# Optimization experiments

Hardware: AMD Instinct MI355X
Metric: run time of the kernel (lower is better)

Reference implementation:

```python
import jax, jax.numpy as jnp
import numpy as np

EPS = 1e-8
CLAMP = 1.0 - 1e-5
C = 1.0  # curvature


def _norm(x):
    return jnp.sqrt(jnp.sum(x * x, axis=-1, keepdims=True))


def clamp_to_ball(x, c=C):
    max_norm = CLAMP / c ** 0.5
    n = jnp.maximum(_norm(x), EPS)
    scale = jnp.where(n > max_norm, max_norm / n, 1.0)
    return x * scale


def logmap0(x, c=C):
    n = jnp.maximum(_norm(x), EPS)
    sc = c ** 0.5
    a = jnp.minimum(sc * n, 1.0 - EPS)
    return jnp.arctanh(a) / (sc * n) * x


def expmap0(v, c=C):
    n = jnp.maximum(_norm(v), EPS)
    sc = c ** 0.5
    t = jnp.minimum(sc * n, 15.0)
    return clamp_to_ball(jnp.tanh(t) * v / (sc * n), c)


def mobius_add(x, y, c=C):
    x2 = jnp.sum(x * x, -1, keepdims=True)
    y2 = jnp.sum(y * y, -1, keepdims=True)
    xy = jnp.sum(x * y, -1, keepdims=True)
    num = (1 + 2 * c * xy + c * y2) * x + (1 - c * x2) * y
    den = 1 + 2 * c * xy + c * c * x2 * y2
    return clamp_to_ball(num / jnp.maximum(den, EPS), c)


def hyp_linear(x, W, b, c=C):
    out = expmap0(logmap0(x, c) @ W.T, c)
    bias_ball = expmap0(b[None, :], c)
    return mobius_add(out, jnp.broadcast_to(bias_ball, out.shape), c)


def pairwise_poincare_dist(Q, K, c=C):
    # Q, K: [B, h, T, dk]. Distance d(q,k) = 2/sqrt(c) * atanh(sqrt(c)*||(-q) (+) k||).
    # ||num||^2 of mobius_add(-q, k) depends only on scalars |q|^2, |k|^2, q.k,
    # so we avoid the (B,h,T,T,dk) expansion while computing identical math.
    q2 = jnp.sum(Q * Q, -1)[..., :, None]          # [B,h,T,1]
    k2 = jnp.sum(K * K, -1)[..., None, :]          # [B,h,1,T]
    xy = -jnp.einsum('bhtd,bhsd->bhts', Q, K)      # (-q).k
    A = 1 + 2 * c * xy + c * k2
    Bc = 1 - c * q2
    num2 = A * A * q2 + Bc * Bc * k2 + 2 * A * Bc * xy
    den = jnp.maximum(1 + 2 * c * xy + c * c * q2 * k2, EPS)
    n = jnp.sqrt(jnp.maximum(num2, 0.0)) / den
    n = jnp.minimum(n, CLAMP / c ** 0.5)           # clamp_to_ball on the diff vector
    n = jnp.minimum(n, 1.0 - EPS)                  # .clamp(max=1-EPS)
    sc = c ** 0.5
    return 2.0 / sc * jnp.arctanh(sc * n)


def setup_inputs() -> dict:
    key = jax.random.key(0)
    ks = jax.random.split(key, 10)
    B, T, d = 4, 1024, 512
    x = expmap0(0.05 * jax.random.normal(ks[0], (B, T, d), jnp.float32))
    a = (6.0 / (d + d)) ** 0.5  # xavier uniform bound
    def w(k):
        return jax.random.uniform(k, (d, d), jnp.float32, -a, a)
    return {
        'x': x,
        'Wq': w(ks[1]), 'bq': 0.01 * jax.random.normal(ks[2], (d,), jnp.float32),
        'Wk': w(ks[3]), 'bk': 0.01 * jax.random.normal(ks[4], (d,), jnp.float32),
        'Wv': w(ks[5]), 'bv': 0.01 * jax.random.normal(ks[6], (d,), jnp.float32),
        'Wo': w(ks[7]), 'bo': 0.01 * jax.random.normal(ks[8], (d,), jnp.float32),
    }


def reference(x, Wq, bq, Wk, bk, Wv, bv, Wo, bo):
    B, T, d = x.shape
    h = 8
    dk = d // h
    x_eucl = logmap0(x, C)
    Q = hyp_linear(x, Wq, bq, C)
    K = hyp_linear(x, Wk, bk, C)
    V = x_eucl @ Wv.T + bv
    Q = Q.reshape(B, T, h, dk).transpose(0, 2, 1, 3)
    K = K.reshape(B, T, h, dk).transpose(0, 2, 1, 3)
    V = V.reshape(B, T, h, dk).transpose(0, 2, 1, 3)
    dists = pairwise_poincare_dist(Q, K, C)        # [B,h,T,T]
    scores = -dists / (dk ** 0.5)
    attn = jax.nn.softmax(scores, axis=-1)
    out = jnp.einsum('bhts,bhsd->bhtd', attn, V)
    out = out.transpose(0, 2, 1, 3).reshape(B, T, d)
    return out @ Wo.T + bo
```

## Files before the change

kernel.cpp:

```cpp
#include <hip/hip_runtime.h>
#include <math.h>

#define EPSF   1e-8f
#define CLAMPF 0.99999f

typedef __attribute__((ext_vector_type(8))) short bf16x8;
typedef __attribute__((ext_vector_type(4))) float f32x4;
#define MFMA16(a,b,c) __builtin_amdgcn_mfma_f32_16x16x32_bf16(a,b,c,0,0,0)

__device__ __forceinline__ unsigned cvt_pk_bf16(float lo, float hi) {
  unsigned r;
  asm("v_cvt_pk_bf16_f32 %0, %1, %2" : "=v"(r) : "v"(lo), "v"(hi));
  return r;
}

__device__ __forceinline__ float wave_sum64(float v) {
  v += __shfl_xor(v, 1, 64);
  v += __shfl_xor(v, 2, 64);
  v += __shfl_xor(v, 4, 64);
  v += __shfl_xor(v, 8, 64);
  v += __shfl_xor(v, 16, 64);
  v += __shfl_xor(v, 32, 64);
  return v;
}

__global__ __launch_bounds__(256) void prep_logmap(const float* __restrict__ x,
                                                   const float* __restrict__ Wq,
                                                   const float* __restrict__ Wk,
                                                   const float* __restrict__ Wv,
                                                   const float* __restrict__ Wo,
                                                   const float* __restrict__ bq,
                                                   const float* __restrict__ bk,
                                                   short* __restrict__ xe,
                                                   short* __restrict__ Wqbf,
                                                   short* __restrict__ Wkbf,
                                                   short* __restrict__ Wvbf,
                                                   short* __restrict__ Wobf,
                                                   float* __restrict__ bb) {
  const int id = blockIdx.x;
  const int t = threadIdx.x;
  __shared__ float red[4];
  if (id < 4096) {
    float2 v = ((const float2*)(x + (size_t)id * 512))[t];
    float s = wave_sum64(v.x * v.x + v.y * v.y);
    if ((t & 63) == 0) red[t >> 6] = s;
    __syncthreads();
    float n2 = red[0] + red[1] + red[2] + red[3];
    float n = sqrtf(n2);
    float nm = fmaxf(n, EPSF);
    float a = fminf(nm, 1.0f);
    float at = 0.5f * logf((1.f + a) / (1.f - a));
    float sc = at / nm;
    ((unsigned*)(xe + (size_t)id * 512))[t] = cvt_pk_bf16(v.x * sc, v.y * sc);
    return;
  }
  const int wid = id - 4096;
  if (wid < 512) {
    const int which = wid >> 7, chunk = wid & 127;
    const float* src; short* dst;
    switch (which) {
      case 0: src = Wq; dst = Wqbf; break;
      case 1: src = Wk; dst = Wkbf; break;
      case 2: src = Wv; dst = Wvbf; break;
      default: src = Wo; dst = Wobf; break;
    }
    const int idx = chunk * 2048 + t * 8;
    float4 a = *(const float4*)(src + idx);
    float4 b2 = *(const float4*)(src + idx + 4);
    union { int4 v; unsigned u[4]; } o;
    o.u[0] = cvt_pk_bf16(a.x, a.y);
    o.u[1] = cvt_pk_bf16(a.z, a.w);
    o.u[2] = cvt_pk_bf16(b2.x, b2.y);
    o.u[3] = cvt_pk_bf16(b2.z, b2.w);
    *(int4*)(dst + idx) = o.v;
    return;
  }
  const int which = wid - 512;
  const float* b = which ? bk : bq;
  float* o = bb + (size_t)which * 520;
  float2 v = ((const float2*)b)[t];
  float s = wave_sum64(v.x * v.x + v.y * v.y);
  if ((t & 63) == 0) red[t >> 6] = s;
  __syncthreads();
  float n2 = red[0] + red[1] + red[2] + red[3];
  float n = sqrtf(n2);
  float nm = fmaxf(n, EPSF);
  float tt = fminf(nm, 15.f);
  float f = tanhf(tt) / nm;
  float on = f * nm;
  if (on > CLAMPF) f *= CLAMPF / on;
  ((float2*)o)[t] = make_float2(f * v.x, f * v.y);
  if (t == 0) o[512] = f * f * n2;
}

template <int VT>
__device__ __forceinline__ void gemm_core(const short* __restrict__ A,
                                          const short* __restrict__ W,
                                          const float* __restrict__ bias,
                                          void* __restrict__ outp,
                                          int bx, int by) {
  __shared__ __align__(16) short As[64][72];
  __shared__ __align__(16) short Ws[64][72];
  const int t = threadIdx.x;
  const int wave = t >> 6, lane = t & 63, lg = lane >> 4, lr = lane & 15;
  const int mh = wave & 1, nh = wave >> 1;
  f32x4 z = {0.f, 0.f, 0.f, 0.f};
  f32x4 acc00 = z, acc01 = z, acc10 = z, acc11 = z;
  const int srow = t >> 2, sc = (t & 3) * 16;
  const short* Ab = A + (size_t)(by * 64 + srow) * 512 + sc;
  const short* Wb = W + (size_t)(bx * 64 + srow) * 512 + sc;

  int4 ra0 = *(const int4*)(Ab);
  int4 ra1 = *(const int4*)(Ab + 8);
  int4 rw0 = *(const int4*)(Wb);
  int4 rw1 = *(const int4*)(Wb + 8);

  for (int kt = 0; kt < 512; kt += 64) {
    __syncthreads();
    *(int4*)&As[srow][sc] = ra0;
    *(int4*)&As[srow][sc + 8] = ra1;
    *(int4*)&Ws[srow][sc] = rw0;
    *(int4*)&Ws[srow][sc + 8] = rw1;
    __syncthreads();
    if (kt < 448) {
      ra0 = *(const int4*)(Ab + kt + 64);
      ra1 = *(const int4*)(Ab + kt + 72);
      rw0 = *(const int4*)(Wb + kt + 64);
      rw1 = *(const int4*)(Wb + kt + 72);
    }
#pragma unroll
    for (int kk = 0; kk < 2; ++kk) {
      bf16x8 af0 = *(const bf16x8*)&As[mh * 32 + lr][kk * 32 + lg * 8];
      bf16x8 af1 = *(const bf16x8*)&As[mh * 32 + 16 + lr][kk * 32 + lg * 8];
      bf16x8 bf0 = *(const bf16x8*)&Ws[nh * 32 + lr][kk * 32 + lg * 8];
      bf16x8 bf1 = *(const bf16x8*)&Ws[nh * 32 + 16 + lr][kk * 32 + lg * 8];
      acc00 = MFMA16(af0, bf0, acc00);
      acc01 = MFMA16(af0, bf1, acc01);
      acc10 = MFMA16(af1, bf0, acc10);
      acc11 = MFMA16(af1, bf1, acc11);
    }
  }

  if (VT == 0) {
    float* out = (float*)outp;
    float b0 = 0.f, b1 = 0.f;
    if (bias) { b0 = bias[bx * 64 + nh * 32 + lr]; b1 = bias[bx * 64 + nh * 32 + 16 + lr]; }
#pragma unroll
    for (int r = 0; r < 4; ++r) {
      size_t row0 = (size_t)(by * 64 + mh * 32 + lg * 4 + r);
      size_t row1 = row0 + 16;
      out[row0 * 512 + bx * 64 + nh * 32 + lr] = acc00[r] + b0;
      out[row0 * 512 + bx * 64 + nh * 32 + 16 + lr] = acc01[r] + b1;
      out[row1 * 512 + bx * 64 + nh * 32 + lr] = acc10[r] + b0;
      out[row1 * 512 + bx * 64 + nh * 32 + 16 + lr] = acc11[r] + b1;
    }
  } else {
    short* vt = (short*)outp;
    const int bidx = by >> 4;
    const int trow0 = (by & 15) * 64 + mh * 32 + lg * 4;
    const int c0 = bx * 64 + nh * 32 + lr;
    const int c1 = c0 + 16;
    const float b0 = bias[c0], b1 = bias[c1];
    size_t base0 = ((size_t)(bidx * 8 + (c0 >> 6)) * 64 + (c0 & 63)) * 1024;
    size_t base1 = ((size_t)(bidx * 8 + (c1 >> 6)) * 64 + (c1 & 63)) * 1024;
    uint2 pk;
    pk.x = cvt_pk_bf16(acc00[0] + b0, acc00[1] + b0);
    pk.y = cvt_pk_bf16(acc00[2] + b0, acc00[3] + b0);
    *(uint2*)(vt + base0 + trow0) = pk;
    pk.x = cvt_pk_bf16(acc01[0] + b1, acc01[1] + b1);
    pk.y = cvt_pk_bf16(acc01[2] + b1, acc01[3] + b1);
    *(uint2*)(vt + base1 + trow0) = pk;
    pk.x = cvt_pk_bf16(acc10[0] + b0, acc10[1] + b0);
    pk.y = cvt_pk_bf16(acc10[2] + b0, acc10[3] + b0);
    *(uint2*)(vt + base0 + trow0 + 16) = pk;
    pk.x = cvt_pk_bf16(acc11[0] + b1, acc11[1] + b1);
    pk.y = cvt_pk_bf16(acc11[2] + b1, acc11[3] + b1);
    *(uint2*)(vt + base1 + trow0 + 16) = pk;
  }
}

__global__ __launch_bounds__(256) void gemm_qkv(const short* __restrict__ A,
                                                const short* __restrict__ Wq,
                                                const short* __restrict__ Wk,
                                                const short* __restrict__ Wv,
                                                const float* __restrict__ bv,
                                                float* __restrict__ Qo,
                                                float* __restrict__ Ko,
                                                short* __restrict__ Vt) {
  switch (blockIdx.z) {
    case 0: gemm_core<0>(A, Wq, nullptr, Qo, blockIdx.x, blockIdx.y); break;
    case 1: gemm_core<0>(A, Wk, nullptr, Ko, blockIdx.x, blockIdx.y); break;
    default: gemm_core<1>(A, Wv, bv, Vt, blockIdx.x, blockIdx.y); break;
  }
}

__global__ __launch_bounds__(256) void gemm_bf(const short* __restrict__ A,
                                               const short* __restrict__ W,
                                               const float* __restrict__ bias,
                                               float* __restrict__ out) {
  gemm_core<0>(A, W, bias, out, blockIdx.x, blockIdx.y);
}

__global__ __launch_bounds__(256) void hyp_epilogue_v3(const float* __restrict__ Qb,
                                                       const float* __restrict__ Kb,
                                                       const float* __restrict__ bbase,
                                                       short* __restrict__ Qbf,
                                                       short* __restrict__ Kbf,
                                                       float* __restrict__ q2h,
                                                       float* __restrict__ k2h) {
  const int row = blockIdx.x;
  const int which = blockIdx.y;
  const float* Y = which ? Kb : Qb;
  const float* bb = bbase + (size_t)which * 520;
  short* Ybf = which ? Kbf : Qbf;
  float* y2h = which ? k2h : q2h;
  const int t = threadIdx.x;
  float2 y = ((const float2*)(Y + (size_t)row * 512))[t];
  float2 w = ((const float2*)bb)[t];
  __shared__ float red[8];
  float sn = wave_sum64(y.x * y.x + y.y * y.y);
  float sd = wave_sum64(y.x * w.x + y.y * w.y);
  if ((t & 63) == 0) { red[t >> 6] = sn; red[4 + (t >> 6)] = sd; }
  __syncthreads();
  float n2 = red[0] + red[1] + red[2] + red[3];
  float dt = red[4] + red[5] + red[6] + red[7];
  float y2 = bb[512];
  float n = sqrtf(n2);
  float nm = fmaxf(n, EPSF);
  float tt = fminf(nm, 15.f);
  float f = tanhf(tt) / nm;
  float on = f * nm;
  if (on > CLAMPF) f *= CLAMPF / on;
  float x2 = f * f * n2;
  float xy = f * dt;
  float A = 1.f + 2.f * xy + y2;
  float Bc = 1.f - x2;
  float den = fmaxf(1.f + 2.f * xy + x2 * y2, EPSF);
  float num2 = A * A * x2 + Bc * Bc * y2 + 2.f * A * Bc * xy;
  float nn = sqrtf(fmaxf(num2, 0.f)) / den;
  float nnm = fmaxf(nn, EPSF);
  float s2 = (nnm > CLAMPF) ? (CLAMPF / nnm) : 1.f;
  float g = s2 / den;
  float ox = g * (A * f * y.x + Bc * w.x);
  float oy = g * (A * f * y.y + Bc * w.y);
  ((unsigned*)(Ybf + (size_t)row * 512))[t] = cvt_pk_bf16(ox, oy);
  float hs = ox * ox + oy * oy;
  hs += __shfl_xor(hs, 1, 64);
  hs += __shfl_xor(hs, 2, 64);
  hs += __shfl_xor(hs, 4, 64);
  hs += __shfl_xor(hs, 8, 64);
  hs += __shfl_xor(hs, 16, 64);
  if ((t & 31) == 0) y2h[(size_t)(t >> 5) * 4096 + row] = hs;
}

__global__ __launch_bounds__(256) void attn_mfma(const short* __restrict__ Qbf,
                                                 const short* __restrict__ Kbf,
                                                 const float* __restrict__ q2h,
                                                 const float* __restrict__ k2h,
                                                 const short* __restrict__ Vt,
                                                 short* __restrict__ Obf) {
  __shared__ __align__(16) short Qs[32][72];
  __shared__ __align__(16) short Ks[64][72];
  __shared__ __align__(16) short Vs[64][72];
  __shared__ __align__(16) short Ps[32][72];
  __shared__ float k2s[64];
  __shared__ float lsl[4][32];

  const int t = threadIdx.x;
  const int id = blockIdx.x;
  const int qt = id >> 5;
  const int pr = (((id >> 3) & 3) << 3) | (id & 7);
  const int hd = pr & 7, b = pr >> 3;

  const int wave = t >> 6, lane = t & 63, lg = lane >> 4, lr = lane & 15;
  const size_t hbase = (size_t)b * 1024 * 512 + (size_t)hd * 64;
  const size_t vtb = (size_t)(b * 8 + hd) * 64 * 1024;
  const int sr = t >> 3, sc8 = (t & 7) * 8;

  *(int4*)&Qs[sr][sc8] = *(const int4*)(Qbf + hbase + (size_t)(qt * 32 + sr) * 512 + sc8);
  __syncthreads();

  bf16x8 qf[2][2];
#pragma unroll
  for (int m = 0; m < 2; ++m)
#pragma unroll
    for (int kk = 0; kk < 2; ++kk)
      qf[m][kk] = *(const bf16x8*)&Qs[m * 16 + lr][kk * 32 + lg * 8];

  float q2m[2], bc2m[2], q2p1m2[2];
#pragma unroll
  for (int m = 0; m < 2; ++m) {
    float q2 = q2h[(size_t)hd * 4096 + b * 1024 + qt * 32 + m * 16 + lr];
    q2m[m] = q2;
    float bc = 1.f - q2;
    bc2m[m] = bc * bc;
    q2p1m2[m] = -2.f * (1.f + q2);
  }

  f32x4 z = {0.f, 0.f, 0.f, 0.f};
  f32x4 accT0 = z, accT1 = z;
  float lsm[2] = {0.f, 0.f};

  const short* kp = Kbf + hbase + (size_t)sr * 512 + sc8;
  const short* vp = Vt + vtb + (size_t)sr * 1024 + sc8;
  const float* k2p = k2h + (size_t)hd * 4096 + b * 1024 + t;

  int4 ka = *(const int4*)kp;
  int4 kb2 = *(const int4*)(kp + 32 * 512);
  int4 va = *(const int4*)vp;
  int4 vb2 = *(const int4*)(vp + 32 * 1024);
  float k2r = 0.f;
  if (t < 64) k2r = *k2p;

  for (int kt = 0; kt < 16; ++kt) {
    __syncthreads();
    *(int4*)&Ks[sr][sc8] = ka;
    *(int4*)&Ks[sr + 32][sc8] = kb2;
    *(int4*)&Vs[sr][sc8] = va;
    *(int4*)&Vs[sr + 32][sc8] = vb2;
    if (t < 64) k2s[t] = k2r;
    __syncthreads();
    if (kt < 15) {
      kp += 64 * 512; vp += 64; k2p += 64;
      ka = *(const int4*)kp;
      kb2 = *(const int4*)(kp + 32 * 512);
      va = *(const int4*)vp;
      vb2 = *(const int4*)(vp + 32 * 1024);
      if (t < 64) k2r = *k2p;
    }

    bf16x8 kf0 = *(const bf16x8*)&Ks[wave * 16 + lr][0 + lg * 8];
    bf16x8 kf1 = *(const bf16x8*)&Ks[wave * 16 + lr][32 + lg * 8];
    f32x4 s0 = z, s1 = z;
    s0 = MFMA16(kf0, qf[0][0], s0);
    s0 = MFMA16(kf1, qf[0][1], s0);
    s1 = MFMA16(kf0, qf[1][0], s1);
    s1 = MFMA16(kf1, qf[1][1], s1);

    float k2v[4], k2p1[4], k2p1sq[4];
#pragma unroll
    for (int r = 0; r < 4; ++r) {
      k2v[r] = k2s[wave * 16 + lg * 4 + r];
      k2p1[r] = 1.f + k2v[r];
      k2p1sq[r] = k2p1[r] * k2p1[r];
    }
#pragma unroll
    for (int m = 0; m < 2; ++m) {
      f32x4 sv = m ? s1 : s0;
      float p[4];
#pragma unroll
      for (int r = 0; r < 4; ++r) {
        float d = sv[r];
        float c1 = q2p1m2[m] * k2p1[r];
        float c0 = fmaf(q2m[m], k2p1sq[r], bc2m[m] * k2v[r]);
        float num2 = fmaf(d, fmaf(4.f, d, c1), c0);
        float den = fmaf(-2.f, d, fmaf(q2m[m], k2v[r], 1.f));
        num2 = fmaxf(num2, 0.f);
        den = fmaxf(den, EPSF);
        float sq = __builtin_amdgcn_sqrtf(num2);
        float u = (den - sq) * __builtin_amdgcn_rcpf(den + sq);
        u = fmaxf(u, 5.000025e-6f);
        p[r] = __builtin_amdgcn_exp2f(0.125f * __builtin_amdgcn_logf(u));
      }
      lsm[m] += (p[0] + p[1]) + (p[2] + p[3]);
      uint2 pk;
      pk.x = cvt_pk_bf16(p[0], p[1]);
      pk.y = cvt_pk_bf16(p[2], p[3]);
      *(uint2*)&Ps[m * 16 + lr][wave * 16 + lg * 4] = pk;
    }
    __syncthreads();

    bf16x8 vf0 = *(const bf16x8*)&Vs[wave * 16 + lr][0 + lg * 8];
    bf16x8 vf1 = *(const bf16x8*)&Vs[wave * 16 + lr][32 + lg * 8];
    bf16x8 pa00 = *(const bf16x8*)&Ps[lr][0 + lg * 8];
    bf16x8 pa01 = *(const bf16x8*)&Ps[lr][32 + lg * 8];
    bf16x8 pa10 = *(const bf16x8*)&Ps[16 + lr][0 + lg * 8];
    bf16x8 pa11 = *(const bf16x8*)&Ps[16 + lr][32 + lg * 8];
    accT0 = MFMA16(vf0, pa00, accT0);
    accT0 = MFMA16(vf1, pa01, accT0);
    accT1 = MFMA16(vf0, pa10, accT1);
    accT1 = MFMA16(vf1, pa11, accT1);
  }

#pragma unroll
  for (int m = 0; m < 2; ++m) {
    float v = lsm[m];
    v += __shfl_xor(v, 16, 64);
    v += __shfl_xor(v, 32, 64);
    lsm[m] = v;
  }
  if (lg == 0) {
    lsl[wave][lr] = lsm[0];
    lsl[wave][16 + lr] = lsm[1];
  }
  __syncthreads();

  float inv0 = 1.f / (lsl[0][lr] + lsl[1][lr] + lsl[2][lr] + lsl[3][lr]);
  float inv1 = 1.f / (lsl[0][16 + lr] + lsl[1][16 + lr] + lsl[2][16 + lr] + lsl[3][16 + lr]);

  short* ob0 = Obf + ((size_t)b * 1024 + qt * 32 + lr) * 512 + hd * 64 + wave * 16 + lg * 4;
  short* ob1 = Obf + ((size_t)b * 1024 + qt * 32 + 16 + lr) * 512 + hd * 64 + wave * 16 + lg * 4;
  *(unsigned*)(ob0)     = cvt_pk_bf16(accT0[0] * inv0, accT0[1] * inv0);
  *(unsigned*)(ob0 + 2) = cvt_pk_bf16(accT0[2] * inv0, accT0[3] * inv0);
  *(unsigned*)(ob1)     = cvt_pk_bf16(accT1[0] * inv1, accT1[1] * inv1);
  *(unsigned*)(ob1 + 2) = cvt_pk_bf16(accT1[2] * inv1, accT1[3] * inv1);
}

extern "C" void kernel_launch(void* const* d_in, const int* in_sizes, int n_in,
                              void* d_out, int out_size, void* d_ws, size_t ws_size,
                              hipStream_t stream) {
  const float* x  = (const float*)d_in[0];
  const float* Wq = (const float*)d_in[1];
  const float* bq = (const float*)d_in[2];
  const float* Wk = (const float*)d_in[3];
  const float* bk = (const float*)d_in[4];
  const float* Wv = (const float*)d_in[5];
  const float* bv = (const float*)d_in[6];
  const float* Wo = (const float*)d_in[7];
  const float* bo = (const float*)d_in[8];
  float* out = (float*)d_out;
  float* ws  = (float*)d_ws;

  const size_t M1 = 1048576ull;
  float* Qb    = ws;
  float* Kb    = ws + 2 * M1;
  short* Vt    = (short*)(ws + 4 * M1);
  short* xe_bf = (short*)(ws + 5 * M1);
  short* Qbf   = (short*)(ws + 5 * M1);
  short* Wqbf  = (short*)(ws + 6 * M1);
  short* Wkbf  = (short*)(ws + 6 * M1 + 131072);
  short* Wvbf  = (short*)(ws + 6 * M1 + 262144);
  short* Wobf  = (short*)(ws + 6 * M1 + 393216);
  short* attn_out = (short*)(ws + 6 * M1 + 524288);
  short* Kbf = (short*)out;
  float* bb  = out + M1;
  float* q2h = out + M1 + 2048;
  float* k2h = out + M1 + 2048 + 32768;

  hipLaunchKernelGGL(prep_logmap, dim3(4610), dim3(256), 0, stream,
                     x, Wq, Wk, Wv, Wo, bq, bk, xe_bf, Wqbf, Wkbf, Wvbf, Wobf, bb);

  hipLaunchKernelGGL(gemm_qkv, dim3(8, 64, 3), dim3(256), 0, stream,
                     xe_bf, Wqbf, Wkbf, Wvbf, bv, Qb, Kb, Vt);

  hipLaunchKernelGGL(hyp_epilogue_v3, dim3(4096, 2), dim3(256), 0, stream,
                     Qb, Kb, bb, Qbf, Kbf, q2h, k2h);

  hipLaunchKernelGGL(attn_mfma, dim3(1024), dim3(256), 0, stream,
                     Qbf, Kbf, q2h, k2h, Vt, attn_out);

  hipLaunchKernelGGL(gemm_bf, dim3(8, 64), dim3(256), 0, stream, attn_out, Wobf, bo, out);
}
```

Before: 82.94 us.

## Restructure attention kernel as register-resident split-K with no shared-memory staging

The attention kernel now gives each wave a 16-row query half and a 512-key half, loads K, V and k2 fragments straight from global memory into registers with one-step prefetch, and feeds the probability tile to the PV MFMA directly from registers through a permuted K row order. This removes the per-iteration LDS staging and the three block barriers per key tile. The two key halves are merged once at the end through shared memory. The cost is redundant global loads across waves, uncoalesced fragment loads, and a final reduction step; launch bounds now ask for 4 blocks per CU.

```diff
diff --git a/kernel.cpp b/kernel.cpp
--- a/kernel.cpp
+++ b/kernel.cpp
@@ -253,157 +253,151 @@
   if ((t & 31) == 0) y2h[(size_t)(t >> 5) * 4096 + row] = hs;
 }
 
-__global__ __launch_bounds__(256) void attn_mfma(const short* __restrict__ Qbf,
-                                                 const short* __restrict__ Kbf,
-                                                 const float* __restrict__ q2h,
-                                                 const float* __restrict__ k2h,
-                                                 const short* __restrict__ Vt,
-                                                 short* __restrict__ Obf) {
-  __shared__ __align__(16) short Qs[32][72];
-  __shared__ __align__(16) short Ks[64][72];
-  __shared__ __align__(16) short Vs[64][72];
-  __shared__ __align__(16) short Ps[32][72];
-  __shared__ float k2s[64];
-  __shared__ float lsl[4][32];
+__global__ __launch_bounds__(256, 4) void attn_mfma_v2(const short* __restrict__ Qbf,
+                                                       const short* __restrict__ Kbf,
+                                                       const float* __restrict__ q2h,
+                                                       const float* __restrict__ k2h,
+                                                       const short* __restrict__ Vt,
+                                                       short* __restrict__ Obf) {
+  __shared__ __align__(16) float Ls[2][16][68];
+  __shared__ float lsb[2][16];
 
   const int t = threadIdx.x;
   const int id = blockIdx.x;
   const int qt = id >> 5;
   const int pr = (((id >> 3) & 3) << 3) | (id & 7);
   const int hd = pr & 7, b = pr >> 3;
-
   const int wave = t >> 6, lane = t & 63, lg = lane >> 4, lr = lane & 15;
-  const size_t hbase = (size_t)b * 1024 * 512 + (size_t)hd * 64;
-  const size_t vtb = (size_t)(b * 8 + hd) * 64 * 1024;
-  const int sr = t >> 3, sc8 = (t & 7) * 8;
-
-  *(int4*)&Qs[sr][sc8] = *(const int4*)(Qbf + hbase + (size_t)(qt * 32 + sr) * 512 + sc8);
-  __syncthreads();
-
-  bf16x8 qf[2][2];
-#pragma unroll
-  for (int m = 0; m < 2; ++m)
-#pragma unroll
-    for (int kk = 0; kk < 2; ++kk)
-      qf[m][kk] = *(const bf16x8*)&Qs[m * 16 + lr][kk * 32 + lg * 8];
-
-  float q2m[2], bc2m[2], q2p1m2[2];
-#pragma unroll
-  for (int m = 0; m < 2; ++m) {
-    float q2 = q2h[(size_t)hd * 4096 + b * 1024 + qt * 32 + m * 16 + lr];
-    q2m[m] = q2;
-    float bc = 1.f - q2;
-    bc2m[m] = bc * bc;
-    q2p1m2[m] = -2.f * (1.f + q2);
-  }
+  const int qh = wave & 1, kh = wave >> 1;
+
+  const size_t qrow = (size_t)(b * 1024 + qt * 32 + qh * 16 + lr);
+  const bf16x8 qf0 = *(const bf16x8*)(Qbf + qrow * 512 + hd * 64 + lg * 8);
+  const bf16x8 qf1 = *(const bf16x8*)(Qbf + qrow * 512 + hd * 64 + 32 + lg * 8);
+
+  const float q2 = q2h[(size_t)hd * 4096 + b * 1024 + qt * 32 + qh * 16 + lr];
+  const float bc = 1.f - q2;
+  const float bc2 = bc * bc;
+  const float q2p1m2 = -2.f * (1.f + q2);
+
+  const int permA = (lr & 3) | ((lr >> 2) << 3);
+  const short* kpA = Kbf + (size_t)(b * 1024 + kh * 512 + permA) * 512 + hd * 64 + lg * 8;
+  const short* kpB = kpA + 4 * 512;
+  const short* vp  = Vt + ((size_t)(b * 8 + hd) * 64 + lr) * 1024 + kh * 512 + lg * 8;
+  const float* c2p = k2h + (size_t)hd * 4096 + b * 1024 + kh * 512 + lg * 8;
 
   f32x4 z = {0.f, 0.f, 0.f, 0.f};
-  f32x4 accT0 = z, accT1 = z;
-  float lsm[2] = {0.f, 0.f};
-
-  const short* kp = Kbf + hbase + (size_t)sr * 512 + sc8;
-  const short* vp = Vt + vtb + (size_t)sr * 1024 + sc8;
-  const float* k2p = k2h + (size_t)hd * 4096 + b * 1024 + t;
-
-  int4 ka = *(const int4*)kp;
-  int4 kb2 = *(const int4*)(kp + 32 * 512);
-  int4 va = *(const int4*)vp;
-  int4 vb2 = *(const int4*)(vp + 32 * 1024);
-  float k2r = 0.f;
-  if (t < 64) k2r = *k2p;
-
-  for (int kt = 0; kt < 16; ++kt) {
-    __syncthreads();
-    *(int4*)&Ks[sr][sc8] = ka;
-    *(int4*)&Ks[sr + 32][sc8] = kb2;
-    *(int4*)&Vs[sr][sc8] = va;
-    *(int4*)&Vs[sr + 32][sc8] = vb2;
-    if (t < 64) k2s[t] = k2r;
-    __syncthreads();
-    if (kt < 15) {
-      kp += 64 * 512; vp += 64; k2p += 64;
-      ka = *(const int4*)kp;
-      kb2 = *(const int4*)(kp + 32 * 512);
-      va = *(const int4*)vp;
-      vb2 = *(const int4*)(vp + 32 * 1024);
-      if (t < 64) k2r = *k2p;
-    }
-
-    bf16x8 kf0 = *(const bf16x8*)&Ks[wave * 16 + lr][0 + lg * 8];
-    bf16x8 kf1 = *(const bf16x8*)&Ks[wave * 16 + lr][32 + lg * 8];
-    f32x4 s0 = z, s1 = z;
-    s0 = MFMA16(kf0, qf[0][0], s0);
-    s0 = MFMA16(kf1, qf[0][1], s0);
-    s1 = MFMA16(kf0, qf[1][0], s1);
-    s1 = MFMA16(kf1, qf[1][1], s1);
-
-    float k2v[4], k2p1[4], k2p1sq[4];
+  f32x4 acc0 = z, acc1 = z, acc2 = z, acc3 = z;
+  float ls = 0.f;
+
+  bf16x8 kA0 = *(const bf16x8*)(kpA);
+  bf16x8 kA1 = *(const bf16x8*)(kpA + 32);
+  bf16x8 kB0 = *(const bf16x8*)(kpB);
+  bf16x8 kB1 = *(const bf16x8*)(kpB + 32);
+  bf16x8 v0 = *(const bf16x8*)(vp);
+  bf16x8 v1 = *(const bf16x8*)(vp + 16 * 1024);
+  bf16x8 v2 = *(const bf16x8*)(vp + 32 * 1024);
+  bf16x8 v3 = *(const bf16x8*)(vp + 48 * 1024);
+  f32x4 c2a = *(const f32x4*)(c2p);
+  f32x4 c2b = *(const f32x4*)(c2p + 4);
+
+  for (int tt = 0; tt < 16; ++tt) {
+    f32x4 sA = MFMA16(kA1, qf1, z);
+    sA = MFMA16(kA0, qf0, sA);
+    f32x4 sB = MFMA16(kB1, qf1, z);
+    sB = MFMA16(kB0, qf0, sB);
+
+    kpA += 32 * 512; kpB += 32 * 512;
+    bf16x8 nA0 = *(const bf16x8*)(kpA);
+    bf16x8 nA1 = *(const bf16x8*)(kpA + 32);
+    bf16x8 nB0 = *(const bf16x8*)(kpB);
+    bf16x8 nB1 = *(const bf16x8*)(kpB + 32);
+
+    float pA[4], pB[4];
 #pragma unroll
     for (int r = 0; r < 4; ++r) {
-      k2v[r] = k2s[wave * 16 + lg * 4 + r];
-      k2p1[r] = 1.f + k2v[r];
-      k2p1sq[r] = k2p1[r] * k2p1[r];
+      float d = sA[r];
+      float k2v = c2a[r];
+      float k2p1 = 1.f + k2v;
+      float c1 = q2p1m2 * k2p1;
+      float c0 = fmaf(q2, k2p1 * k2p1, bc2 * k2v);
+      float num2 = fmaxf(fmaf(d, fmaf(4.f, d, c1), c0), 0.f);
+      float den = fmaxf(fmaf(-2.f, d, fmaf(q2, k2v, 1.f)), EPSF);
+      float sq = __builtin_amdgcn_sqrtf(num2);
+      float u = fmaxf((den - sq) * __builtin_amdgcn_rcpf(den + sq), 5.000025e-6f);
+      pA[r] = __builtin_amdgcn_exp2f(0.125f * __builtin_amdgcn_logf(u));
     }
 #pragma unroll
-    for (int m = 0; m < 2; ++m) {
-      f32x4 sv = m ? s1 : s0;
-      float p[4];
-#pragma unroll
-      for (int r = 0; r < 4; ++r) {
-        float d = sv[r];
-        float c1 = q2p1m2[m] * k2p1[r];
-        float c0 = fmaf(q2m[m], k2p1sq[r], bc2m[m] * k2v[r]);
-        float num2 = fmaf(d, fmaf(4.f, d, c1), c0);
-        float den = fmaf(-2.f, d, fmaf(q2m[m], k2v[r], 1.f));
-        num2 = fmaxf(num2, 0.f);
-        den = fmaxf(den, EPSF);
-        float sq = __builtin_amdgcn_sqrtf(num2);
-        float u = (den - sq) * __builtin_amdgcn_rcpf(den + sq);
-        u = fmaxf(u, 5.000025e-6f);
-        p[r] = __builtin_amdgcn_exp2f(0.125f * __builtin_amdgcn_logf(u));
-      }
-      lsm[m] += (p[0] + p[1]) + (p[2] + p[3]);
-      uint2 pk;
-      pk.x = cvt_pk_bf16(p[0], p[1]);
-      pk.y = cvt_pk_bf16(p[2], p[3]);
-      *(uint2*)&Ps[m * 16 + lr][wave * 16 + lg * 4] = pk;
-    }
-    __syncthreads();
-
-    bf16x8 vf0 = *(const bf16x8*)&Vs[wave * 16 + lr][0 + lg * 8];
-    bf16x8 vf1 = *(const bf16x8*)&Vs[wave * 16 + lr][32 + lg * 8];
-    bf16x8 pa00 = *(const bf16x8*)&Ps[lr][0 + lg * 8];
-    bf16x8 pa01 = *(const bf16x8*)&Ps[lr][32 + lg * 8];
-    bf16x8 pa10 = *(const bf16x8*)&Ps[16 + lr][0 + lg * 8];
-    bf16x8 pa11 = *(const bf16x8*)&Ps[16 + lr][32 + lg * 8];
-    accT0 = MFMA16(vf0, pa00, accT0);
-    accT0 = MFMA16(vf1, pa01, accT0);
-    accT1 = MFMA16(vf0, pa10, accT1);
-    accT1 = MFMA16(vf1, pa11, accT1);
-  }
-
-#pragma unroll
-  for (int m = 0; m < 2; ++m) {
-    float v = lsm[m];
-    v += __shfl_xor(v, 16, 64);
-    v += __shfl_xor(v, 32, 64);
-    lsm[m] = v;
-  }
-  if (lg == 0) {
-    lsl[wave][lr] = lsm[0];
-    lsl[wave][16 + lr] = lsm[1];
+    for (int r = 0; r < 4; ++r) {
+      float d = sB[r];
+      float k2v = c2b[r];
+      float k2p1 = 1.f + k2v;
+      float c1 = q2p1m2 * k2p1;
+      float c0 = fmaf(q2, k2p1 * k2p1, bc2 * k2v);
+      float num2 = fmaxf(fmaf(d, fmaf(4.f, d, c1), c0), 0.f);
+      float den = fmaxf(fmaf(-2.f, d, fmaf(q2, k2v, 1.f)), EPSF);
+      float sq = __builtin_amdgcn_sqrtf(num2);
+      float u = fmaxf((den - sq) * __builtin_amdgcn_rcpf(den + sq), 5.000025e-6f);
+      pB[r] = __builtin_amdgcn_exp2f(0.125f * __builtin_amdgcn_logf(u));
+    }
+    ls += (pA[0] + pA[1] + pA[2] + pA[3]) + (pB[0] + pB[1] + pB[2] + pB[3]);
+
+    c2p += 32;
+    f32x4 nc2a = *(const f32x4*)(c2p);
+    f32x4 nc2b = *(const f32x4*)(c2p + 4);
+
+    union { unsigned u[4]; bf16x8 v; } pf;
+    pf.u[0] = cvt_pk_bf16(pA[0], pA[1]);
+    pf.u[1] = cvt_pk_bf16(pA[2], pA[3]);
+    pf.u[2] = cvt_pk_bf16(pB[0], pB[1]);
+    pf.u[3] = cvt_pk_bf16(pB[2], pB[3]);
+
+    acc0 = MFMA16(v0, pf.v, acc0);
+    acc1 = MFMA16(v1, pf.v, acc1);
+    acc2 = MFMA16(v2, pf.v, acc2);
+    acc3 = MFMA16(v3, pf.v, acc3);
+
+    vp += 32;
+    v0 = *(const bf16x8*)(vp);
+    v1 = *(const bf16x8*)(vp + 16 * 1024);
+    v2 = *(const bf16x8*)(vp + 32 * 1024);
+    v3 = *(const bf16x8*)(vp + 48 * 1024);
+
+    kA0 = nA0; kA1 = nA1; kB0 = nB0; kB1 = nB1;
+    c2a = nc2a; c2b = nc2b;
+  }
+
+  ls += __shfl_xor(ls, 16, 64);
+  ls += __shfl_xor(ls, 32, 64);
+
+  if (kh == 1) {
+    *(f32x4*)&Ls[qh][lr][lg * 4]      = acc0;
+    *(f32x4*)&Ls[qh][lr][16 + lg * 4] = acc1;
+    *(f32x4*)&Ls[qh][lr][32 + lg * 4] = acc2;
+    *(f32x4*)&Ls[qh][lr][48 + lg * 4] = acc3;
+    if (lg == 0) lsb[qh][lr] = ls;
   }
   __syncthreads();
-
-  float inv0 = 1.f / (lsl[0][lr] + lsl[1][lr] + lsl[2][lr] + lsl[3][lr]);
-  float inv1 = 1.f / (lsl[0][16 + lr] + lsl[1][16 + lr] + lsl[2][16 + lr] + lsl[3][16 + lr]);
-
-  short* ob0 = Obf + ((size_t)b * 1024 + qt * 32 + lr) * 512 + hd * 64 + wave * 16 + lg * 4;
-  short* ob1 = Obf + ((size_t)b * 1024 + qt * 32 + 16 + lr) * 512 + hd * 64 + wave * 16 + lg * 4;
-  *(unsigned*)(ob0)     = cvt_pk_bf16(accT0[0] * inv0, accT0[1] * inv0);
-  *(unsigned*)(ob0 + 2) = cvt_pk_bf16(accT0[2] * inv0, accT0[3] * inv0);
-  *(unsigned*)(ob1)     = cvt_pk_bf16(accT1[0] * inv1, accT1[1] * inv1);
-  *(unsigned*)(ob1 + 2) = cvt_pk_bf16(accT1[2] * inv1, accT1[3] * inv1);
+  if (kh == 0) {
+    acc0 += *(const f32x4*)&Ls[qh][lr][lg * 4];
+    acc1 += *(const f32x4*)&Ls[qh][lr][16 + lg * 4];
+    acc2 += *(const f32x4*)&Ls[qh][lr][32 + lg * 4];
+    acc3 += *(const f32x4*)&Ls[qh][lr][48 + lg * 4];
+    float inv = 1.f / (ls + lsb[qh][lr]);
+    short* ob = Obf + qrow * 512 + hd * 64 + lg * 4;
+    uint2 pk;
+    pk.x = cvt_pk_bf16(acc0[0] * inv, acc0[1] * inv);
+    pk.y = cvt_pk_bf16(acc0[2] * inv, acc0[3] * inv);
+    *(uint2*)(ob) = pk;
+    pk.x = cvt_pk_bf16(acc1[0] * inv, acc1[1] * inv);
+    pk.y = cvt_pk_bf16(acc1[2] * inv, acc1[3] * inv);
+    *(uint2*)(ob + 16) = pk;
+    pk.x = cvt_pk_bf16(acc2[0] * inv, acc2[1] * inv);
+    pk.y = cvt_pk_bf16(acc2[2] * inv, acc2[3] * inv);
+    *(uint2*)(ob + 32) = pk;
+    pk.x = cvt_pk_bf16(acc3[0] * inv, acc3[1] * inv);
+    pk.y = cvt_pk_bf16(acc3[2] * inv, acc3[3] * inv);
+    *(uint2*)(ob + 48) = pk;
+  }
 }
 
 extern "C" void kernel_launch(void* const* d_in, const int* in_sizes, int n_in,
@@ -446,7 +440,7 @@
   hipLaunchKernelGGL(hyp_epilogue_v3, dim3(4096, 2), dim3(256), 0, stream,
                      Qb, Kb, bb, Qbf, Kbf, q2h, k2h);
 
-  hipLaunchKernelGGL(attn_mfma, dim3(1024), dim3(256), 0, stream,
+  hipLaunchKernelGGL(attn_mfma_v2, dim3(1024), dim3(256), 0, stream,
                      Qbf, Kbf, q2h, k2h, Vt, attn_out);
 
   hipLaunchKernelGGL(gemm_bf, dim3(8, 64), dim3(256), 0, stream, attn_out, Wobf, bo, out);
```

Measured after the change: 110.2 us. 32.9% more time.
